# Performance work log

Measured on AMD Instinct MI355X. Metric: run time of the kernel, lower is better.

The kernel has to match this reference:

```python
import jax, jax.numpy as jnp
import numpy as np

N = 100000      # nodes
E = 1600000     # edges
IN_FEATS = 128
HIDDEN = 64
NUM_GRAPHS = 512
BN_EPS = 1e-5


def setup_inputs() -> dict:
    key = jax.random.key(0)
    ks = jax.random.split(key, 20)
    x = jax.random.normal(ks[0], (N, IN_FEATS), dtype=jnp.float32)
    edge_index = jax.random.randint(ks[1], (2, E), 0, N, dtype=jnp.int64)
    batch = jnp.sort(jax.random.randint(ks[2], (N,), 0, NUM_GRAPHS, dtype=jnp.int64))
    def lin(k, fin, fout):
        k1, k2 = jax.random.split(k)
        s = 1.0 / np.sqrt(fin)
        W = jax.random.uniform(k1, (fout, fin), minval=-s, maxval=s, dtype=jnp.float32)
        b = jax.random.uniform(k2, (fout,), minval=-s, maxval=s, dtype=jnp.float32)
        return W, b
    W1a, b1a = lin(ks[3], IN_FEATS, HIDDEN)
    W1b, b1b = lin(ks[4], HIDDEN, HIDDEN)
    W2a, b2a = lin(ks[5], HIDDEN, HIDDEN)
    W2b, b2b = lin(ks[6], HIDDEN, HIDDEN)
    def bn(k):
        k1, k2, k3, k4 = jax.random.split(k, 4)
        g = jax.random.uniform(k1, (HIDDEN,), minval=0.5, maxval=1.5, dtype=jnp.float32)
        be = jax.random.normal(k2, (HIDDEN,), dtype=jnp.float32) * 0.1
        m = jax.random.normal(k3, (HIDDEN,), dtype=jnp.float32) * 0.1
        v = jax.random.uniform(k4, (HIDDEN,), minval=0.5, maxval=1.5, dtype=jnp.float32)
        return g, be, m, v
    g1, be1, m1, v1 = bn(ks[7])
    g2, be2, m2, v2 = bn(ks[8])
    return dict(x=x, edge_index=edge_index, batch=batch,
                W1a=W1a, b1a=b1a, W1b=W1b, b1b=b1b, g1=g1, be1=be1, m1=m1, v1=v1,
                W2a=W2a, b2a=b2a, W2b=W2b, b2b=b2b, g2=g2, be2=be2, m2=m2, v2=v2)


def _gin_layer(x, src, dst, Wa, ba, Wb, bb):
    # sum-aggregate neighbor features: gather at src, scatter-add to dst
    agg = jax.ops.segment_sum(x[src], dst, num_segments=N)
    h = x + agg  # eps = 0 default in PyG GINConv
    h = jax.nn.relu(h @ Wa.T + ba)
    return h @ Wb.T + bb


def _bn_eval(x, g, be, m, v):
    return (x - m) * (g * jax.lax.rsqrt(v + BN_EPS)) + be


def reference(x, edge_index, batch,
              W1a, b1a, W1b, b1b, g1, be1, m1, v1,
              W2a, b2a, W2b, b2b, g2, be2, m2, v2):
    src, dst = edge_index[0], edge_index[1]
    h = jax.nn.relu(_bn_eval(_gin_layer(x, src, dst, W1a, b1a, W1b, b1b), g1, be1, m1, v1))
    # dropout identity (eval)
    h = jax.nn.relu(_bn_eval(_gin_layer(h, src, dst, W2a, b2a, W2b, b2b), g2, be2, m2, v2))
    # global mean pool by graph id
    sums = jax.ops.segment_sum(h, batch, num_segments=NUM_GRAPHS)
    counts = jax.ops.segment_sum(jnp.ones((N,), dtype=h.dtype), batch, num_segments=NUM_GRAPHS)
    return sums / jnp.maximum(counts, 1.0)[:, None]
```

## Files before the change

### kernel.cpp

```cpp
#include <hip/hip_runtime.h>

#define BN_EPS 1e-5f
#define CHUNK 4096
#define MAXB 512

typedef __attribute__((ext_vector_type(8))) short short8v;
typedef __attribute__((ext_vector_type(4))) float f32x4;

__device__ __forceinline__ unsigned short f2bf(float f) {
    unsigned int u = __float_as_uint(f);
    u += 0x7FFF + ((u >> 16) & 1);
    return (unsigned short)(u >> 16);
}
__device__ __forceinline__ float bf2f(unsigned short h) {
    return __uint_as_float((unsigned int)h << 16);
}
__device__ __forceinline__ float bflo(unsigned int u) { return __uint_as_float(u << 16); }
__device__ __forceinline__ float bfhi(unsigned int u) { return __uint_as_float(u & 0xffff0000u); }

__device__ __forceinline__ short8v pack8(const float* f) {
    short8v r;
#pragma unroll
    for (int i = 0; i < 8; i++) r[i] = (short)f2bf(f[i]);
    return r;
}


__global__ __launch_bounds__(256) void bin_count(const int* __restrict__ ei, int E,
                                                 int* __restrict__ bcnt, int nbuck) {
    __shared__ int h[MAXB];
    for (int i = threadIdx.x; i < nbuck; i += 256) h[i] = 0;
    __syncthreads();
    int i = blockIdx.x * 256 + threadIdx.x, stride = gridDim.x * 256;
    for (int e = i; e < E; e += stride) {
        int d = ei[E + e];
        atomicAdd(&h[d >> 8], 1);
    }
    __syncthreads();
    for (int b = threadIdx.x; b < nbuck; b += 256)
        if (h[b]) atomicAdd(&bcnt[b], h[b]);
}

__global__ __launch_bounds__(512) void scan_small(const int* __restrict__ bcnt,
                                                  int* __restrict__ boff,
                                                  int* __restrict__ bpos,
                                                  int* __restrict__ row_ptr_end,
                                                  int nbuck, int E) {
    __shared__ int wsum[8];
    int tid = threadIdx.x, lane = tid & 63, wv = tid >> 6;
    int val = (tid < nbuck) ? bcnt[tid] : 0;
    int s = val;
#pragma unroll
    for (int off = 1; off < 64; off <<= 1) {
        int t = __shfl_up(s, off, 64);
        if (lane >= off) s += t;
    }
    if (lane == 63) wsum[wv] = s;
    __syncthreads();
    if (wv == 0) {
        int t = (lane < 8) ? wsum[lane] : 0;
#pragma unroll
        for (int off = 1; off < 8; off <<= 1) {
            int u = __shfl_up(t, off, 64);
            if (lane >= off) t += u;
        }
        if (lane < 8) wsum[lane] = t;
    }
    __syncthreads();
    int excl = ((wv == 0) ? 0 : wsum[wv - 1]) + s - val;
    if (tid < nbuck) { boff[tid] = excl; bpos[tid] = excl; }
    if (tid == 0) { boff[nbuck] = E; *row_ptr_end = E; }
}

__global__ __launch_bounds__(256) void bin_scatter(const int* __restrict__ ei, int E,
                                                   int* __restrict__ bpos,
                                                   int* __restrict__ binned, int nbuck) {
    __shared__ int h[MAXB];
    __shared__ int res[MAXB];
    int base = blockIdx.x * CHUNK;
    int cnt = min(CHUNK, E - base);
    int tid = threadIdx.x;
    for (int b = tid; b < nbuck; b += 256) h[b] = 0;
    __syncthreads();
    for (int k = tid; k < cnt; k += 256) {
        int d = ei[E + base + k];
        atomicAdd(&h[d >> 8], 1);
    }
    __syncthreads();
    for (int b = tid; b < nbuck; b += 256) {
        int c = h[b];
        res[b] = c ? atomicAdd(&bpos[b], c) : 0;
        h[b] = 0;
    }
    __syncthreads();
    for (int k = tid; k < cnt; k += 256) {
        int srcv = ei[base + k];
        int d = ei[E + base + k];
        int b = d >> 8;
        int r = atomicAdd(&h[b], 1);
        binned[res[b] + r] = ((d & 255) << 17) | srcv;
    }
}

__global__ __launch_bounds__(256) void bucket_csr(const int* __restrict__ binned,
                                                  const int* __restrict__ boff,
                                                  int* __restrict__ row_ptr,
                                                  int* __restrict__ esrc, int N) {
    __shared__ int ncnt[256];
    __shared__ int npos[256];
    __shared__ int wsum[4];
    int b = blockIdx.x, tid = threadIdx.x, lane = tid & 63, wv = tid >> 6;
    int lo = boff[b], hi = boff[b + 1];
    int base_node = b << 8;
    ncnt[tid] = 0;
    __syncthreads();
    for (int i = lo + tid; i < hi; i += 256)
        atomicAdd(&ncnt[binned[i] >> 17], 1);
    __syncthreads();
    int c = ncnt[tid];
    int s = c;
#pragma unroll
    for (int off = 1; off < 64; off <<= 1) {
        int t = __shfl_up(s, off, 64);
        if (lane >= off) s += t;
    }
    if (lane == 63) wsum[wv] = s;
    __syncthreads();
    int woff = 0;
#pragma unroll
    for (int i = 0; i < 4; i++) woff += (i < wv) ? wsum[i] : 0;
    int abspos = lo + woff + (s - c);
    if (base_node + tid < N) row_ptr[base_node + tid] = abspos;
    npos[tid] = abspos;
    __syncthreads();
    for (int i = lo + tid; i < hi; i += 256) {
        int val = binned[i];
        int r = atomicAdd(&npos[val >> 17], 1);
        esrc[r] = val & 0x1FFFF;
    }
}


__global__ __launch_bounds__(256) void linear_mfma(const float* __restrict__ X,
                                                   const float* __restrict__ W,
                                                   unsigned short* __restrict__ Y, int N) {
    __shared__ short8v al[16 * 16];
    int tid = threadIdx.x, wv = tid >> 6, lane = tid & 63;
    int lr = lane & 15, lh = lane >> 4;
    short8v bw[4];
    {
        const float* wrow = W + (size_t)(wv * 16 + lr) * 128;
#pragma unroll
        for (int kk = 0; kk < 4; kk++) {
            float tmp[8];
            *(float4*)tmp = *(const float4*)(wrow + kk * 32 + lh * 8);
            *(float4*)(tmp + 4) = *(const float4*)(wrow + kk * 32 + lh * 8 + 4);
            bw[kk] = pack8(tmp);
        }
    }
    unsigned short* yb = Y + (size_t)wv * N * 16 + lr;
    int r = tid >> 4, s = tid & 15;
    for (int nb = blockIdx.x * 16; nb < N; nb += gridDim.x * 16) {
        const float* xg = X + (size_t)(nb + r) * 128 + s * 8;
        float tmp[8];
        *(float4*)tmp = *(const float4*)xg;
        *(float4*)(tmp + 4) = *(const float4*)(xg + 4);
        al[r * 16 + (s ^ r)] = pack8(tmp);
        __syncthreads();
        f32x4 acc = {0.f, 0.f, 0.f, 0.f};
#pragma unroll
        for (int kk = 0; kk < 4; kk++) {
            short8v a = al[lr * 16 + ((kk * 4 + lh) ^ lr)];
            acc = __builtin_amdgcn_mfma_f32_16x16x32_bf16(a, bw[kk], acc, 0, 0, 0);
        }
#pragma unroll
        for (int ri = 0; ri < 4; ri++)
            yb[(size_t)(nb + lh * 4 + ri) * 16] = f2bf(acc[ri]);
        __syncthreads();
    }
}

__global__ __launch_bounds__(256) void mlp1_mfma(const unsigned short* __restrict__ T,
        const float* __restrict__ W, const float* __restrict__ b,
        const float* __restrict__ g, const float* __restrict__ be,
        const float* __restrict__ m, const float* __restrict__ v,
        unsigned short* __restrict__ H, int N) {
    __shared__ short8v al[16 * 8];
    int tid = threadIdx.x, wv = tid >> 6, lane = tid & 63;
    int lr = lane & 15, lh = lane >> 4;
    short8v bw[2];
    {
        const float* wrow = W + (size_t)(wv * 16 + lr) * 64;
#pragma unroll
        for (int kk = 0; kk < 2; kk++) {
            float tmp[8];
            *(float4*)tmp = *(const float4*)(wrow + kk * 32 + lh * 8);
            *(float4*)(tmp + 4) = *(const float4*)(wrow + kk * 32 + lh * 8 + 4);
            bw[kk] = pack8(tmp);
        }
    }
    int col = wv * 16 + lr;
    float bias = b[col];
    float sc = g[col] * rsqrtf(v[col] + BN_EPS);
    float cc = be[col] - m[col] * sc;
    int rr = tid >> 3, ss = tid & 7;
    for (int nb = blockIdx.x * 16; nb < N; nb += gridDim.x * 16) {
        if (tid < 128) {
            const short8v* tg = (const short8v*)(T + (size_t)(nb + rr) * 64);
            al[rr * 8 + (ss ^ (rr & 7))] = tg[ss];
        }
        __syncthreads();
        f32x4 acc = {0.f, 0.f, 0.f, 0.f};
#pragma unroll
        for (int kk = 0; kk < 2; kk++) {
            short8v a = al[lr * 8 + ((kk * 4 + lh) ^ (lr & 7))];
            acc = __builtin_amdgcn_mfma_f32_16x16x32_bf16(a, bw[kk], acc, 0, 0, 0);
        }
        unsigned short* hb = H + (size_t)nb * 64 + col;
#pragma unroll
        for (int ri = 0; ri < 4; ri++) {
            float o = fmaxf((acc[ri] + bias) * sc + cc, 0.f);
            hb[(size_t)(lh * 4 + ri) * 64] = f2bf(o);
        }
        __syncthreads();
    }
}

__global__ __launch_bounds__(256) void mlp2_mfma(const unsigned short* __restrict__ T,
        const float* __restrict__ W1, const float* __restrict__ b1,
        const float* __restrict__ g, const float* __restrict__ be,
        const float* __restrict__ m, const float* __restrict__ v,
        const float* __restrict__ W2, unsigned short* __restrict__ Y, int N) {
    __shared__ short8v al[16 * 8];
    __shared__ short8v hl[16 * 8];
    int tid = threadIdx.x, wv = tid >> 6, lane = tid & 63;
    int lr = lane & 15, lh = lane >> 4;
    short8v bw1[2], bw2[2];
    {
        const float* w1r = W1 + (size_t)(wv * 16 + lr) * 64;
        const float* w2r = W2 + (size_t)(wv * 16 + lr) * 64;
#pragma unroll
        for (int kk = 0; kk < 2; kk++) {
            float tmp[8];
            *(float4*)tmp = *(const float4*)(w1r + kk * 32 + lh * 8);
            *(float4*)(tmp + 4) = *(const float4*)(w1r + kk * 32 + lh * 8 + 4);
            bw1[kk] = pack8(tmp);
            *(float4*)tmp = *(const float4*)(w2r + kk * 32 + lh * 8);
            *(float4*)(tmp + 4) = *(const float4*)(w2r + kk * 32 + lh * 8 + 4);
            bw2[kk] = pack8(tmp);
        }
    }
    int col = wv * 16 + lr;
    float bias = b1[col];
    float sc = g[col] * rsqrtf(v[col] + BN_EPS);
    float cc = be[col] - m[col] * sc;
    unsigned short* hu = (unsigned short*)hl;
    unsigned short* yb = Y + (size_t)wv * N * 16 + lr;
    int rr = tid >> 3, ss = tid & 7;
    for (int nb = blockIdx.x * 16; nb < N; nb += gridDim.x * 16) {
        if (tid < 128) {
            const short8v* tg = (const short8v*)(T + (size_t)(nb + rr) * 64);
            al[rr * 8 + (ss ^ (rr & 7))] = tg[ss];
        }
        __syncthreads();
        f32x4 acc = {0.f, 0.f, 0.f, 0.f};
#pragma unroll
        for (int kk = 0; kk < 2; kk++) {
            short8v a = al[lr * 8 + ((kk * 4 + lh) ^ (lr & 7))];
            acc = __builtin_amdgcn_mfma_f32_16x16x32_bf16(a, bw1[kk], acc, 0, 0, 0);
        }
#pragma unroll
        for (int ri = 0; ri < 4; ri++) {
            float o = fmaxf((acc[ri] + bias) * sc + cc, 0.f);
            int row = lh * 4 + ri;
            int slot = (col >> 3) ^ (row & 7);
            hu[(row * 8 + slot) * 8 + (col & 7)] = f2bf(o);
        }
        __syncthreads();
        f32x4 acc2 = {0.f, 0.f, 0.f, 0.f};
#pragma unroll
        for (int kk = 0; kk < 2; kk++) {
            short8v a = hl[lr * 8 + ((kk * 4 + lh) ^ (lr & 7))];
            acc2 = __builtin_amdgcn_mfma_f32_16x16x32_bf16(a, bw2[kk], acc2, 0, 0, 0);
        }
#pragma unroll
        for (int ri = 0; ri < 4; ri++)
            yb[(size_t)(nb + lh * 4 + ri) * 16] = f2bf(acc2[ri]);
        __syncthreads();
    }
}

__global__ __launch_bounds__(256) void gather_plane(const unsigned short* __restrict__ Yp,
        const int* __restrict__ row_ptr, const int* __restrict__ esrc,
        const float* __restrict__ bias, unsigned short* __restrict__ T, int N) {
    int b = blockIdx.x;
    int p = b & 3;
    int g = b >> 2;
    int wv = threadIdx.x >> 6, lane = threadIdx.x & 63;
    int half = lane & 1, slot = (lane >> 1) & 7, nsub = lane >> 4;
    int node = g * 16 + wv * 4 + nsub;
    bool valid = node < N;
    int nd = valid ? node : 0;
    int e0 = row_ptr[nd];
    int e1 = valid ? row_ptr[nd + 1] : e0;
    int la = max(e1 - 1, 0);
    const uint4* Yh = (const uint4*)(Yp + (size_t)p * N * 16);
    int eb0 = e0 + slot, eb1 = eb0 + 8, eb2 = eb0 + 16, eb3 = eb0 + 24;
    int s0 = esrc[min(eb0, la)];
    int s1 = esrc[min(eb1, la)];
    int s2 = esrc[min(eb2, la)];
    int s3 = esrc[min(eb3, la)];
    uint4 q0 = Yh[s0 * 2 + half];
    uint4 q1 = Yh[s1 * 2 + half];
    uint4 q2 = Yh[s2 * 2 + half];
    uint4 q3 = Yh[s3 * 2 + half];
    bool k0 = eb0 < e1, k1 = eb1 < e1, k2 = eb2 < e1, k3 = eb3 < e1;
    q0.x = k0 ? q0.x : 0u; q0.y = k0 ? q0.y : 0u; q0.z = k0 ? q0.z : 0u; q0.w = k0 ? q0.w : 0u;
    q1.x = k1 ? q1.x : 0u; q1.y = k1 ? q1.y : 0u; q1.z = k1 ? q1.z : 0u; q1.w = k1 ? q1.w : 0u;
    q2.x = k2 ? q2.x : 0u; q2.y = k2 ? q2.y : 0u; q2.z = k2 ? q2.z : 0u; q2.w = k2 ? q2.w : 0u;
    q3.x = k3 ? q3.x : 0u; q3.y = k3 ? q3.y : 0u; q3.z = k3 ? q3.z : 0u; q3.w = k3 ? q3.w : 0u;
    float a0 = (bflo(q0.x) + bflo(q1.x)) + (bflo(q2.x) + bflo(q3.x));
    float a1 = (bfhi(q0.x) + bfhi(q1.x)) + (bfhi(q2.x) + bfhi(q3.x));
    float a2 = (bflo(q0.y) + bflo(q1.y)) + (bflo(q2.y) + bflo(q3.y));
    float a3 = (bfhi(q0.y) + bfhi(q1.y)) + (bfhi(q2.y) + bfhi(q3.y));
    float a4 = (bflo(q0.z) + bflo(q1.z)) + (bflo(q2.z) + bflo(q3.z));
    float a5 = (bfhi(q0.z) + bfhi(q1.z)) + (bfhi(q2.z) + bfhi(q3.z));
    float a6 = (bflo(q0.w) + bflo(q1.w)) + (bflo(q2.w) + bflo(q3.w));
    float a7 = (bfhi(q0.w) + bfhi(q1.w)) + (bfhi(q2.w) + bfhi(q3.w));
    for (int e = e0 + 32 + slot; e < e1; e += 8) {
        int s = esrc[e];
        uint4 q = Yh[s * 2 + half];
        a0 += bflo(q.x); a1 += bfhi(q.x);
        a2 += bflo(q.y); a3 += bfhi(q.y);
        a4 += bflo(q.z); a5 += bfhi(q.z);
        a6 += bflo(q.w); a7 += bfhi(q.w);
    }
#pragma unroll
    for (int off = 2; off <= 8; off <<= 1) {
        a0 += __shfl_xor(a0, off, 64);
        a1 += __shfl_xor(a1, off, 64);
        a2 += __shfl_xor(a2, off, 64);
        a3 += __shfl_xor(a3, off, 64);
        a4 += __shfl_xor(a4, off, 64);
        a5 += __shfl_xor(a5, off, 64);
        a6 += __shfl_xor(a6, off, 64);
        a7 += __shfl_xor(a7, off, 64);
    }
    if (slot == 0 && valid) {
        uint4 qs = Yh[node * 2 + half];
        const float4* bp = (const float4*)(bias + p * 16 + half * 8);
        float4 bl = bp[0];
        float4 bh = bp[1];
        a0 += bflo(qs.x) + bl.x; a1 += bfhi(qs.x) + bl.y;
        a2 += bflo(qs.y) + bl.z; a3 += bfhi(qs.y) + bl.w;
        a4 += bflo(qs.z) + bh.x; a5 += bfhi(qs.z) + bh.y;
        a6 += bflo(qs.w) + bh.z; a7 += bfhi(qs.w) + bh.w;
        uint4 o;
        o.x = (unsigned int)f2bf(fmaxf(a0, 0.f)) | ((unsigned int)f2bf(fmaxf(a1, 0.f)) << 16);
        o.y = (unsigned int)f2bf(fmaxf(a2, 0.f)) | ((unsigned int)f2bf(fmaxf(a3, 0.f)) << 16);
        o.z = (unsigned int)f2bf(fmaxf(a4, 0.f)) | ((unsigned int)f2bf(fmaxf(a5, 0.f)) << 16);
        o.w = (unsigned int)f2bf(fmaxf(a6, 0.f)) | ((unsigned int)f2bf(fmaxf(a7, 0.f)) << 16);
        *(uint4*)(T + (size_t)node * 64 + p * 16 + half * 8) = o;
    }
}

__global__ __launch_bounds__(256) void pool_kernel(const unsigned short* __restrict__ H,
                                                   const int* __restrict__ batch,
                                                   float* __restrict__ out, int N) {
    __shared__ float part[4][64];
    int g = blockIdx.x;
    int tid = threadIdx.x, wv = tid >> 6, lane = tid & 63;
    int lo = 0, hi = N;
    while (lo < hi) { int mid = (lo + hi) >> 1; if (batch[mid] < g) lo = mid + 1; else hi = mid; }
    int start = lo;
    hi = N;
    while (lo < hi) { int mid = (lo + hi) >> 1; if (batch[mid] < g + 1) lo = mid + 1; else hi = mid; }
    int end = lo;
    float acc = 0.f;
    for (int i = start + wv; i < end; i += 4) acc += bf2f(H[(size_t)i * 64 + lane]);
    part[wv][lane] = acc;
    __syncthreads();
    if (tid < 64) {
        float sfin = part[0][tid] + part[1][tid] + part[2][tid] + part[3][tid];
        float cnt = (float)(end - start);
        out[(size_t)g * 64 + tid] = sfin / fmaxf(cnt, 1.f);
    }
}

extern "C" void kernel_launch(void* const* d_in, const int* in_sizes, int n_in,
                              void* d_out, int out_size, void* d_ws, size_t ws_size,
                              hipStream_t stream) {
    const float* x   = (const float*)d_in[0];
    const int*   ei  = (const int*)d_in[1];
    const int*   bat = (const int*)d_in[2];
    const float* W1a = (const float*)d_in[3];
    const float* b1a = (const float*)d_in[4];
    const float* W1b = (const float*)d_in[5];
    const float* b1b = (const float*)d_in[6];
    const float* g1  = (const float*)d_in[7];
    const float* be1 = (const float*)d_in[8];
    const float* m1  = (const float*)d_in[9];
    const float* v1  = (const float*)d_in[10];
    const float* W2a = (const float*)d_in[11];
    const float* b2a = (const float*)d_in[12];
    const float* W2b = (const float*)d_in[13];
    const float* b2b = (const float*)d_in[14];
    const float* g2  = (const float*)d_in[15];
    const float* be2 = (const float*)d_in[16];
    const float* m2  = (const float*)d_in[17];
    const float* v2  = (const float*)d_in[18];
    float* out = (float*)d_out;

    int N = in_sizes[0] / 128;
    int E = in_sizes[1] / 2;
    int G = out_size / 64;
    int nbuck = (N + 255) >> 8;

    char* ws = (char*)d_ws;
    int* row_ptr = (int*)ws;
    int* bcnt = row_ptr + ((N + 1 + 3) & ~3);
    int* boff = bcnt + MAXB;
    int* bpos = boff + MAXB + 4;
    int* esrc = bpos + MAXB;
    unsigned short* bufA = (unsigned short*)(esrc + E);
    unsigned short* bufB = bufA + (size_t)N * 64;
    int* binned = (int*)bufB;

    hipMemsetAsync(bcnt, 0, MAXB * sizeof(int), stream);
    bin_count<<<512, 256, 0, stream>>>(ei, E, bcnt, nbuck);
    scan_small<<<1, 512, 0, stream>>>(bcnt, boff, bpos, row_ptr + N, nbuck, E);
    bin_scatter<<<(E + CHUNK - 1) / CHUNK, 256, 0, stream>>>(ei, E, bpos, binned, nbuck);
    bucket_csr<<<nbuck, 256, 0, stream>>>(binned, boff, row_ptr, esrc, N);

    int ngb = (N + 15) / 16;

    linear_mfma<<<2048, 256, 0, stream>>>(x, W1a, bufA, N);
    gather_plane<<<4 * ngb, 256, 0, stream>>>(bufA, row_ptr, esrc, b1a, bufB, N);
    mlp2_mfma<<<2048, 256, 0, stream>>>(bufB, W1b, b1b, g1, be1, m1, v1, W2a, bufA, N);

    gather_plane<<<4 * ngb, 256, 0, stream>>>(bufA, row_ptr, esrc, b2a, bufB, N);
    mlp1_mfma<<<2048, 256, 0, stream>>>(bufB, W2b, b2b, g2, be2, m2, v2, bufA, N);

    pool_kernel<<<G, 256, 0, stream>>>(bufA, bat, out, N);
}
```

Measured before the change: 347.4 us.

## Fuse mean-pool into final MLP via atomics and predicate gather loads

The final MLP kernel now accumulates its post-BN ReLU outputs straight into the pooled output with float atomicAdd per node row, instead of writing a bf16 activation buffer that a separate pool kernel reads back. A small finalize kernel then divides by per-graph node counts, and the output is zeroed with a memset first. The gather kernel also makes its first four neighbor loads conditional rather than loading and masking them. This removes one N x 64 write and read, but adds many atomics to contended addresses, since nodes are sorted by graph, and makes the summation order nondeterministic.

```diff
diff --git a/kernel.cpp b/kernel.cpp
--- a/kernel.cpp
+++ b/kernel.cpp
@@ -180,11 +180,11 @@
     }
 }
 
-__global__ __launch_bounds__(256) void mlp1_mfma(const unsigned short* __restrict__ T,
+__global__ __launch_bounds__(256) void mlp1_pool_mfma(const unsigned short* __restrict__ T,
         const float* __restrict__ W, const float* __restrict__ b,
         const float* __restrict__ g, const float* __restrict__ be,
         const float* __restrict__ m, const float* __restrict__ v,
-        unsigned short* __restrict__ H, int N) {
+        const int* __restrict__ bat, float* __restrict__ out, int N) {
     __shared__ short8v al[16 * 8];
     int tid = threadIdx.x, wv = tid >> 6, lane = tid & 63;
     int lr = lane & 15, lh = lane >> 4;
@@ -216,14 +216,27 @@
             short8v a = al[lr * 8 + ((kk * 4 + lh) ^ (lr & 7))];
             acc = __builtin_amdgcn_mfma_f32_16x16x32_bf16(a, bw[kk], acc, 0, 0, 0);
         }
-        unsigned short* hb = H + (size_t)nb * 64 + col;
 #pragma unroll
         for (int ri = 0; ri < 4; ri++) {
             float o = fmaxf((acc[ri] + bias) * sc + cc, 0.f);
-            hb[(size_t)(lh * 4 + ri) * 64] = f2bf(o);
-        }
-        __syncthreads();
-    }
+            int row = nb + lh * 4 + ri;
+            int gi = bat[row];
+            atomicAdd(&out[(size_t)gi * 64 + col], o);
+        }
+        __syncthreads();
+    }
+}
+
+__global__ __launch_bounds__(64) void finalize_pool(const int* __restrict__ batch,
+                                                    float* __restrict__ out, int N) {
+    int g = blockIdx.x;
+    int lo = 0, hi = N;
+    while (lo < hi) { int mid = (lo + hi) >> 1; if (batch[mid] < g) lo = mid + 1; else hi = mid; }
+    int start = lo;
+    hi = N;
+    while (lo < hi) { int mid = (lo + hi) >> 1; if (batch[mid] < g + 1) lo = mid + 1; else hi = mid; }
+    float inv = 1.f / fmaxf((float)(lo - start), 1.f);
+    out[(size_t)g * 64 + threadIdx.x] *= inv;
 }
 
 __global__ __launch_bounds__(256) void mlp2_mfma(const unsigned short* __restrict__ T,
@@ -310,15 +323,12 @@
     int s1 = esrc[min(eb1, la)];
     int s2 = esrc[min(eb2, la)];
     int s3 = esrc[min(eb3, la)];
-    uint4 q0 = Yh[s0 * 2 + half];
-    uint4 q1 = Yh[s1 * 2 + half];
-    uint4 q2 = Yh[s2 * 2 + half];
-    uint4 q3 = Yh[s3 * 2 + half];
-    bool k0 = eb0 < e1, k1 = eb1 < e1, k2 = eb2 < e1, k3 = eb3 < e1;
-    q0.x = k0 ? q0.x : 0u; q0.y = k0 ? q0.y : 0u; q0.z = k0 ? q0.z : 0u; q0.w = k0 ? q0.w : 0u;
-    q1.x = k1 ? q1.x : 0u; q1.y = k1 ? q1.y : 0u; q1.z = k1 ? q1.z : 0u; q1.w = k1 ? q1.w : 0u;
-    q2.x = k2 ? q2.x : 0u; q2.y = k2 ? q2.y : 0u; q2.z = k2 ? q2.z : 0u; q2.w = k2 ? q2.w : 0u;
-    q3.x = k3 ? q3.x : 0u; q3.y = k3 ? q3.y : 0u; q3.z = k3 ? q3.z : 0u; q3.w = k3 ? q3.w : 0u;
+    uint4 q0 = {0u, 0u, 0u, 0u}, q1 = {0u, 0u, 0u, 0u};
+    uint4 q2 = {0u, 0u, 0u, 0u}, q3 = {0u, 0u, 0u, 0u};
+    if (eb0 < e1) q0 = Yh[s0 * 2 + half];
+    if (eb1 < e1) q1 = Yh[s1 * 2 + half];
+    if (eb2 < e1) q2 = Yh[s2 * 2 + half];
+    if (eb3 < e1) q3 = Yh[s3 * 2 + half];
     float a0 = (bflo(q0.x) + bflo(q1.x)) + (bflo(q2.x) + bflo(q3.x));
     float a1 = (bfhi(q0.x) + bfhi(q1.x)) + (bfhi(q2.x) + bfhi(q3.x));
     float a2 = (bflo(q0.y) + bflo(q1.y)) + (bflo(q2.y) + bflo(q3.y));
@@ -361,29 +371,6 @@
         o.z = (unsigned int)f2bf(fmaxf(a4, 0.f)) | ((unsigned int)f2bf(fmaxf(a5, 0.f)) << 16);
         o.w = (unsigned int)f2bf(fmaxf(a6, 0.f)) | ((unsigned int)f2bf(fmaxf(a7, 0.f)) << 16);
         *(uint4*)(T + (size_t)node * 64 + p * 16 + half * 8) = o;
-    }
-}
-
-__global__ __launch_bounds__(256) void pool_kernel(const unsigned short* __restrict__ H,
-                                                   const int* __restrict__ batch,
-                                                   float* __restrict__ out, int N) {
-    __shared__ float part[4][64];
-    int g = blockIdx.x;
-    int tid = threadIdx.x, wv = tid >> 6, lane = tid & 63;
-    int lo = 0, hi = N;
-    while (lo < hi) { int mid = (lo + hi) >> 1; if (batch[mid] < g) lo = mid + 1; else hi = mid; }
-    int start = lo;
-    hi = N;
-    while (lo < hi) { int mid = (lo + hi) >> 1; if (batch[mid] < g + 1) lo = mid + 1; else hi = mid; }
-    int end = lo;
-    float acc = 0.f;
-    for (int i = start + wv; i < end; i += 4) acc += bf2f(H[(size_t)i * 64 + lane]);
-    part[wv][lane] = acc;
-    __syncthreads();
-    if (tid < 64) {
-        float sfin = part[0][tid] + part[1][tid] + part[2][tid] + part[3][tid];
-        float cnt = (float)(end - start);
-        out[(size_t)g * 64 + tid] = sfin / fmaxf(cnt, 1.f);
     }
 }
 
@@ -427,6 +414,7 @@
     int* binned = (int*)bufB;
 
     hipMemsetAsync(bcnt, 0, MAXB * sizeof(int), stream);
+    hipMemsetAsync(out, 0, out_size, stream);
     bin_count<<<512, 256, 0, stream>>>(ei, E, bcnt, nbuck);
     scan_small<<<1, 512, 0, stream>>>(bcnt, boff, bpos, row_ptr + N, nbuck, E);
     bin_scatter<<<(E + CHUNK - 1) / CHUNK, 256, 0, stream>>>(ei, E, bpos, binned, nbuck);
@@ -439,7 +427,7 @@
     mlp2_mfma<<<2048, 256, 0, stream>>>(bufB, W1b, b1b, g1, be1, m1, v1, W2a, bufA, N);
 
     gather_plane<<<4 * ngb, 256, 0, stream>>>(bufA, row_ptr, esrc, b2a, bufB, N);
-    mlp1_mfma<<<2048, 256, 0, stream>>>(bufB, W2b, b2b, g2, be2, m2, v2, bufA, N);
-
-    pool_kernel<<<G, 256, 0, stream>>>(bufA, bat, out, N);
-}
+    mlp1_pool_mfma<<<2048, 256, 0, stream>>>(bufB, W2b, b2b, g2, be2, m2, v2, bat, out, N);
+
+    finalize_pool<<<G, 64, 0, stream>>>(bat, out, N);
+}
```

New measurement: 499.1 us. 1.44x slower.
